# Optimization experiments

Measured on AMD Instinct MI355X. Metric: run time of the kernel, lower is better.

The kernel has to match this reference:

```python
import jax, jax.numpy as jnp
import numpy as np

EMBED_DIM = 4096
LOW_RANK = 512
BATCH = 8192
K_SEL = 128


def setup_inputs() -> dict:
    key = jax.random.key(0)
    k1, k2, k3, k4 = jax.random.split(key, 4)
    base = jax.random.normal(k1, (BATCH, EMBED_DIM), dtype=jnp.float32)
    source = jax.random.normal(k2, (BATCH, EMBED_DIM), dtype=jnp.float32)
    # fast path: only subspaces[0] is used (all examples share the same index set)
    row = jax.random.randint(k3, (1, K_SEL), 0, LOW_RANK)
    subspaces = jnp.broadcast_to(row, (BATCH, K_SEL)).astype(jnp.int64)
    # orthogonal (column-orthonormal) rotation weight, as produced by
    # torch.nn.utils.parametrizations.orthogonal on [embed_dim, low_rank]
    W, _ = jnp.linalg.qr(jax.random.normal(k4, (EMBED_DIM, LOW_RANK), dtype=jnp.float32))
    return {"base": base, "source": source, "subspaces": subspaces, "W": W}


def reference(base, source, subspaces, W):
    # rotated_base / rotated_source: [B, r]
    # diff in rotated space, gather selected subspace columns, project back.
    sel = subspaces[0]                      # [k] shared index set (fast path)
    diff = (source - base) @ W              # [B, r]
    diff_sel = diff[:, sel]                 # [B, k]
    W_sel = W[:, sel]                       # [d, k]
    out = base + diff_sel @ W_sel.T         # [B, d]
    return out.astype(base.dtype)
```

## Files before the change

### kernel.cpp

```cpp
#include <hip/hip_runtime.h>
#include <hip/hip_bf16.h>

typedef __attribute__((ext_vector_type(4))) float  f32x4;
typedef __attribute__((ext_vector_type(8))) short  short8;

#define EMBED 4096
#define LR    512
#define KSEL  128
#define BATCH 8192
#define NSLICE 8
#define KSLICE 512

__device__ __forceinline__ short f2bf(float x) {
  union { float f; unsigned u; } c; c.f = x;
  unsigned r = c.u + 0x7FFFu + ((c.u >> 16) & 1u);
  return (short)(r >> 16);
}
__device__ __forceinline__ float bf2f(short s) {
  union { unsigned u; float f; } c; c.u = ((unsigned)(unsigned short)s) << 16;
  return c.f;
}
__device__ __forceinline__ void storept(float* p, float v) { *p = v; }
__device__ __forceinline__ void storept(short* p, float v) { *p = f2bf(v); }
__device__ __forceinline__ void loadpart(const float* p, f32x4& a, f32x4& b) {
  a += *(const f32x4*)p; b += *(const f32x4*)(p + 4);
}
__device__ __forceinline__ void loadpart(const short* p, f32x4& a, f32x4& b) {
  short8 v = *(const short8*)p;
  #pragma unroll
  for (int j = 0; j < 4; ++j) { a[j] += bf2f(v[j]); b[j] += bf2f(v[4 + j]); }
}

__global__ __launch_bounds__(256) void pack_w_kernel(
    const float* __restrict__ W, const int* __restrict__ sel,
    short* __restrict__ Wp, short* __restrict__ Wtp) {
  int idx = blockIdx.x * 256 + threadIdx.x;
  int e = idx >> 7;
  int c = idx & 127;
  int r = sel[c];
  short v = f2bf(W[e * LR + r]);
  Wp [(((e >> 3) << 7) + c) * 8 + (e & 7)] = v;
  Wtp[(((c >> 3) << 12) + e) * 8 + (c & 7)] = v;
}

template<typename PT>
__global__ __launch_bounds__(512, 4) void gemm1a_kernel(
    const float* __restrict__ base, const float* __restrict__ src,
    const short* __restrict__ Wp, PT* __restrict__ Tpart) {
  const int t  = threadIdx.x;
  const int w  = t >> 6, l = t & 63;
  const int lr = l & 15, lg = l >> 4;
  const int rg = blockIdx.x & 63, slice = blockIdx.x >> 6;
  const int row0 = rg * 128 + w * 16;
  const int k0 = slice * KSLICE;

  const float* bp = base + (size_t)(row0 + lr) * EMBED + k0 + lg * 8;
  const float* sp = src  + (size_t)(row0 + lr) * EMBED + k0 + lg * 8;
  const short8* wq = (const short8*)Wp + ((k0 >> 3) + lg) * 128 + lr;

  f32x4 acc[8];
  #pragma unroll
  for (int c = 0; c < 8; ++c) acc[c] = (f32x4){0.f, 0.f, 0.f, 0.f};

  #pragma unroll
  for (int ks = 0; ks < 16; ++ks) {
    f32x4 b0 = *(const f32x4*)(bp + ks * 32);
    f32x4 b1 = *(const f32x4*)(bp + ks * 32 + 4);
    f32x4 s0 = *(const f32x4*)(sp + ks * 32);
    f32x4 s1 = *(const f32x4*)(sp + ks * 32 + 4);
    union { short8 v; __hip_bfloat162 h[4]; } ua;
    ua.h[0] = __float22bfloat162_rn(make_float2(s0[0] - b0[0], s0[1] - b0[1]));
    ua.h[1] = __float22bfloat162_rn(make_float2(s0[2] - b0[2], s0[3] - b0[3]));
    ua.h[2] = __float22bfloat162_rn(make_float2(s1[0] - b1[0], s1[1] - b1[1]));
    ua.h[3] = __float22bfloat162_rn(make_float2(s1[2] - b1[2], s1[3] - b1[3]));
    #pragma unroll
    for (int c = 0; c < 8; ++c) {
      short8 bf = wq[ks * 512 + c * 16];
      acc[c] = __builtin_amdgcn_mfma_f32_16x16x32_bf16(ua.v, bf, acc[c], 0, 0, 0);
    }
  }

  PT* o = Tpart + ((size_t)slice * BATCH + row0 + lg * 4) * KSEL + lr;
  #pragma unroll
  for (int c = 0; c < 8; ++c)
    #pragma unroll
    for (int r = 0; r < 4; ++r)
      storept(o + (size_t)r * KSEL + c * 16, acc[c][r]);
}

template<typename PT>
__global__ __launch_bounds__(512) void reduce_kernel(
    const PT* __restrict__ Tpart, short* __restrict__ Tp) {
  const int tid = blockIdx.x * 512 + threadIdx.x;
  const int kkg = tid & 15, row = tid >> 4;
  f32x4 s0 = {0.f, 0.f, 0.f, 0.f}, s1 = {0.f, 0.f, 0.f, 0.f};
  #pragma unroll
  for (int s = 0; s < NSLICE; ++s)
    loadpart(Tpart + ((size_t)s * BATCH + row) * KSEL + kkg * 8, s0, s1);
  short8 o;
  #pragma unroll
  for (int j = 0; j < 4; ++j) { o[j] = f2bf(s0[j]); o[4 + j] = f2bf(s1[j]); }
  *(short8*)(Tp + ((size_t)kkg * BATCH + row) * 8) = o;
}

__global__ __launch_bounds__(256) void gemm2_kernel(
    const float* __restrict__ base, const short* __restrict__ Tp,
    const short* __restrict__ Wtp, float* __restrict__ out) {
  const int t  = threadIdx.x;
  const int w  = t >> 6, l = t & 63;
  const int lr = l & 15, lg = l >> 4;
  const int mt = blockIdx.x >> 4, nt = blockIdx.x & 15;
  const int row0 = mt * 64;
  const int col0 = nt * 256 + w * 64;

  short8 afr[4][4];
  #pragma unroll
  for (int m = 0; m < 4; ++m)
    #pragma unroll
    for (int ks = 0; ks < 4; ++ks)
      afr[m][ks] = *(const short8*)(Tp + (size_t)(((ks * 4 + lg) << 13) + row0 + m * 16 + lr) * 8);

  f32x4 acc[4][4];
  #pragma unroll
  for (int m = 0; m < 4; ++m)
    #pragma unroll
    for (int nf = 0; nf < 4; ++nf) acc[m][nf] = (f32x4){0.f, 0.f, 0.f, 0.f};

  #pragma unroll
  for (int nf = 0; nf < 4; ++nf) {
    short8 bfr[4];
    #pragma unroll
    for (int ks = 0; ks < 4; ++ks)
      bfr[ks] = *(const short8*)(Wtp + (size_t)(((ks * 4 + lg) << 12) + col0 + nf * 16 + lr) * 8);
    #pragma unroll
    for (int m = 0; m < 4; ++m)
      #pragma unroll
      for (int ks = 0; ks < 4; ++ks)
        acc[m][nf] = __builtin_amdgcn_mfma_f32_16x16x32_bf16(afr[m][ks], bfr[ks], acc[m][nf], 0, 0, 0);
  }

  #pragma unroll
  for (int m = 0; m < 4; ++m)
    #pragma unroll
    for (int r = 0; r < 4; ++r) {
      const size_t row = row0 + m * 16 + lg * 4 + r;
      #pragma unroll
      for (int nf = 0; nf < 4; ++nf) {
        const size_t o = row * EMBED + col0 + nf * 16 + lr;
        out[o] = base[o] + acc[m][nf][r];
      }
    }
}

extern "C" void kernel_launch(void* const* d_in, const int* in_sizes, int n_in,
                              void* d_out, int out_size, void* d_ws, size_t ws_size,
                              hipStream_t stream) {
  const float* base = (const float*)d_in[0];
  const float* src  = (const float*)d_in[1];
  const int*   sub  = (const int*)d_in[2];
  const float* W    = (const float*)d_in[3];
  float* out = (float*)d_out;

  short* Wp  = (short*)d_ws;
  short* Wtp = Wp  + EMBED * KSEL;
  short* Tp  = Wtp + EMBED * KSEL;
  char*  rest = (char*)(Tp + BATCH * KSEL);

  pack_w_kernel<<<EMBED * KSEL / 256, 256, 0, stream>>>(W, sub, Wp, Wtp);

  const size_t need_f32 = (size_t)4 * 1024 * 1024 +
                          (size_t)NSLICE * BATCH * KSEL * sizeof(float);
  if (ws_size >= need_f32) {
    float* Tpart = (float*)rest;
    gemm1a_kernel<float><<<512, 512, 0, stream>>>(base, src, Wp, Tpart);
    reduce_kernel<float><<<BATCH * 16 / 512, 512, 0, stream>>>(Tpart, Tp);
  } else {
    short* Tpart = (short*)rest;
    gemm1a_kernel<short><<<512, 512, 0, stream>>>(base, src, Wp, Tpart);
    reduce_kernel<short><<<BATCH * 16 / 512, 512, 0, stream>>>(Tpart, Tp);
  }

  gemm2_kernel<<<(BATCH / 64) * 16, 256, 0, stream>>>(base, Tp, Wtp, out);
}
```

Baseline: 142.7 us.

## Stage gemm1 operands through LDS with double-buffered async global-to-LDS loads

Rewrites the first GEMM kernel so base, source and packed W tiles are copied into shared memory with global_load_lds in a two-stage double buffer, using an XOR swizzle to avoid bank conflicts. The block tile becomes 64 rows by 128 columns across 4 waves in a 2x2 layout, and the grid grows to 1024 blocks of 256 threads with slice-major block ordering. The aim is to overlap HBM loads with MFMA work and to share W fragments through LDS instead of each wave reloading them from global memory. The cost is 48KB of LDS per block, which may limit occupancy, plus a barrier on every k-step.

```diff
diff --git a/kernel.cpp b/kernel.cpp
--- a/kernel.cpp
+++ b/kernel.cpp
@@ -3,6 +3,7 @@
 
 typedef __attribute__((ext_vector_type(4))) float  f32x4;
 typedef __attribute__((ext_vector_type(8))) short  short8;
+typedef unsigned int u32;
 
 #define EMBED 4096
 #define LR    512
@@ -29,6 +30,10 @@
   short8 v = *(const short8*)p;
   #pragma unroll
   for (int j = 0; j < 4; ++j) { a[j] += bf2f(v[j]); b[j] += bf2f(v[4 + j]); }
+}
+__device__ __forceinline__ void gload16(const void* g, void* l) {
+  __builtin_amdgcn_global_load_lds((const __attribute__((address_space(1))) u32*)g,
+                                   (__attribute__((address_space(3))) u32*)l, 16, 0, 0);
 }
 
 __global__ __launch_bounds__(256) void pack_w_kernel(
@@ -44,48 +49,88 @@
 }
 
 template<typename PT>
-__global__ __launch_bounds__(512, 4) void gemm1a_kernel(
+__global__ __launch_bounds__(256, 4) void gemm1a_kernel(
     const float* __restrict__ base, const float* __restrict__ src,
     const short* __restrict__ Wp, PT* __restrict__ Tpart) {
+  __shared__ __align__(16) char smem[49152];
   const int t  = threadIdx.x;
   const int w  = t >> 6, l = t & 63;
   const int lr = l & 15, lg = l >> 4;
-  const int rg = blockIdx.x & 63, slice = blockIdx.x >> 6;
-  const int row0 = rg * 128 + w * 16;
+  const int wm = w >> 1, wn = w & 1;
+  const int slice = blockIdx.x & 7, tile = blockIdx.x >> 3;
+  const int row0 = tile * 64;
   const int k0 = slice * KSLICE;
 
-  const float* bp = base + (size_t)(row0 + lr) * EMBED + k0 + lg * 8;
-  const float* sp = src  + (size_t)(row0 + lr) * EMBED + k0 + lg * 8;
-  const short8* wq = (const short8*)Wp + ((k0 >> 3) + lg) * 128 + lr;
-
-  f32x4 acc[8];
-  #pragma unroll
-  for (int c = 0; c < 8; ++c) acc[c] = (f32x4){0.f, 0.f, 0.f, 0.f};
-
-  #pragma unroll
-  for (int ks = 0; ks < 16; ++ks) {
-    f32x4 b0 = *(const f32x4*)(bp + ks * 32);
-    f32x4 b1 = *(const f32x4*)(bp + ks * 32 + 4);
-    f32x4 s0 = *(const f32x4*)(sp + ks * 32);
-    f32x4 s1 = *(const f32x4*)(sp + ks * 32 + 4);
-    union { short8 v; __hip_bfloat162 h[4]; } ua;
-    ua.h[0] = __float22bfloat162_rn(make_float2(s0[0] - b0[0], s0[1] - b0[1]));
-    ua.h[1] = __float22bfloat162_rn(make_float2(s0[2] - b0[2], s0[3] - b0[3]));
-    ua.h[2] = __float22bfloat162_rn(make_float2(s1[0] - b1[0], s1[1] - b1[1]));
-    ua.h[3] = __float22bfloat162_rn(make_float2(s1[2] - b1[2], s1[3] - b1[3]));
-    #pragma unroll
-    for (int c = 0; c < 8; ++c) {
-      short8 bf = wq[ks * 512 + c * 16];
-      acc[c] = __builtin_amdgcn_mfma_f32_16x16x32_bf16(ua.v, bf, acc[c], 0, 0, 0);
+  const int r_q0 = t >> 3,          c_q0 = t & 7;
+  const int r_q1 = (t + 256) >> 3,  c_q1 = t & 7;
+  const size_t aoff0 = (size_t)(row0 + r_q0) * EMBED + k0 + ((c_q0 ^ (r_q0 & 7)) << 2);
+  const size_t aoff1 = (size_t)(row0 + r_q1) * EMBED + k0 + ((c_q1 ^ (r_q1 & 7)) << 2);
+  const short* bsrc = Wp + ((size_t)(k0 >> 3) * 128 + t) * 8;
+
+  #define STAGE(s, b) do {                                              \
+    char* d_ = smem + (b) * 24576 + t * 16;                             \
+    gload16(base + aoff0 + (s) * 32, d_);                               \
+    gload16(base + aoff1 + (s) * 32, d_ + 4096);                        \
+    gload16(src  + aoff0 + (s) * 32, d_ + 8192);                        \
+    gload16(src  + aoff1 + (s) * 32, d_ + 12288);                       \
+    gload16(bsrc + (s) * 4096,        d_ + 16384);                      \
+    gload16(bsrc + (s) * 4096 + 2048, d_ + 20480);                      \
+  } while (0)
+
+  f32x4 acc[2][4];
+  #pragma unroll
+  for (int m = 0; m < 2; ++m)
+    #pragma unroll
+    for (int n = 0; n < 4; ++n) acc[m][n] = (f32x4){0.f, 0.f, 0.f, 0.f};
+
+  const int row_m0 = wm * 32 + lr;
+  const int row_m1 = wm * 32 + 16 + lr;
+  const int a00 = row_m0 * 128 + (((lg << 1))     ^ (row_m0 & 7)) * 16;
+  const int a01 = row_m0 * 128 + (((lg << 1) | 1) ^ (row_m0 & 7)) * 16;
+  const int a10 = row_m1 * 128 + (((lg << 1))     ^ (row_m1 & 7)) * 16;
+  const int a11 = row_m1 * 128 + (((lg << 1) | 1) ^ (row_m1 & 7)) * 16;
+  const int bofs = 16384 + (lg * 128 + wn * 64 + lr) * 16;
+
+  STAGE(0, 0);
+  int b = 0;
+  for (int s = 0; s < 16; ++s) {
+    __syncthreads();
+    if (s < 15) STAGE(s + 1, b ^ 1);
+    const char* tb = smem + b * 24576;
+
+    short8 ua[2];
+    #pragma unroll
+    for (int m = 0; m < 2; ++m) {
+      const int o0 = m ? a10 : a00, o1 = m ? a11 : a01;
+      f32x4 b0 = *(const f32x4*)(tb + o0);
+      f32x4 b1 = *(const f32x4*)(tb + o1);
+      f32x4 s0 = *(const f32x4*)(tb + 8192 + o0);
+      f32x4 s1 = *(const f32x4*)(tb + 8192 + o1);
+      union { short8 v; __hip_bfloat162 h[4]; } u;
+      u.h[0] = __float22bfloat162_rn(make_float2(s0[0] - b0[0], s0[1] - b0[1]));
+      u.h[1] = __float22bfloat162_rn(make_float2(s0[2] - b0[2], s0[3] - b0[3]));
+      u.h[2] = __float22bfloat162_rn(make_float2(s1[0] - b1[0], s1[1] - b1[1]));
+      u.h[3] = __float22bfloat162_rn(make_float2(s1[2] - b1[2], s1[3] - b1[3]));
+      ua[m] = u.v;
     }
+    #pragma unroll
+    for (int n = 0; n < 4; ++n) {
+      short8 bf = *(const short8*)(tb + bofs + n * 256);
+      acc[0][n] = __builtin_amdgcn_mfma_f32_16x16x32_bf16(ua[0], bf, acc[0][n], 0, 0, 0);
+      acc[1][n] = __builtin_amdgcn_mfma_f32_16x16x32_bf16(ua[1], bf, acc[1][n], 0, 0, 0);
+    }
+    b ^= 1;
   }
-
-  PT* o = Tpart + ((size_t)slice * BATCH + row0 + lg * 4) * KSEL + lr;
-  #pragma unroll
-  for (int c = 0; c < 8; ++c)
-    #pragma unroll
-    for (int r = 0; r < 4; ++r)
-      storept(o + (size_t)r * KSEL + c * 16, acc[c][r]);
+  #undef STAGE
+
+  PT* o = Tpart + ((size_t)slice * BATCH + row0 + wm * 32 + lg * 4) * KSEL + wn * 64 + lr;
+  #pragma unroll
+  for (int m = 0; m < 2; ++m)
+    #pragma unroll
+    for (int n = 0; n < 4; ++n)
+      #pragma unroll
+      for (int r = 0; r < 4; ++r)
+        storept(o + ((size_t)m * 16 + r) * KSEL + n * 16, acc[m][n][r]);
 }
 
 template<typename PT>
@@ -172,11 +217,11 @@
                           (size_t)NSLICE * BATCH * KSEL * sizeof(float);
   if (ws_size >= need_f32) {
     float* Tpart = (float*)rest;
-    gemm1a_kernel<float><<<512, 512, 0, stream>>>(base, src, Wp, Tpart);
+    gemm1a_kernel<float><<<1024, 256, 0, stream>>>(base, src, Wp, Tpart);
     reduce_kernel<float><<<BATCH * 16 / 512, 512, 0, stream>>>(Tpart, Tp);
   } else {
     short* Tpart = (short*)rest;
-    gemm1a_kernel<short><<<512, 512, 0, stream>>>(base, src, Wp, Tpart);
+    gemm1a_kernel<short><<<1024, 256, 0, stream>>>(base, src, Wp, Tpart);
     reduce_kernel<short><<<BATCH * 16 / 512, 512, 0, stream>>>(Tpart, Tp);
   }
 
```

Measured after the change: 129.4 us. -9.3%, faster.
